# Performance work log

Hardware: AMD Instinct MI355X
Metric: run time of the kernel (lower is better)

The kernel has to match this reference:

```python
import jax, jax.numpy as jnp
import numpy as np

FEATURE_DIM = 128
HIDDEN_DIM = 128
BATCH = 500000
NEG_SLOPE = 0.2  # PyG GATConv default negative_slope


def setup_inputs() -> dict:
    key = jax.random.key(0)
    ks = jax.random.split(key, 8)
    s_in = 1.0 / np.sqrt(FEATURE_DIM)
    s_hid = 1.0 / np.sqrt(HIDDEN_DIM)
    return {
        "feature1": jax.random.normal(ks[0], (BATCH, FEATURE_DIM), jnp.float32),
        "feature2": jax.random.normal(ks[1], (BATCH, FEATURE_DIM), jnp.float32),
        # GATConv params (heads=1): lin (no bias), att_src/att_dst, output bias
        "W_gat": jax.random.normal(ks[2], (HIDDEN_DIM, FEATURE_DIM), jnp.float32) * s_in,
        "att_src": jax.random.normal(ks[3], (HIDDEN_DIM,), jnp.float32) * s_hid,
        "att_dst": jax.random.normal(ks[4], (HIDDEN_DIM,), jnp.float32) * s_hid,
        "b_gat": jnp.zeros((HIDDEN_DIM,), jnp.float32),
        # fc: Linear(hidden_dim, feature_dim)
        "W_fc": jax.random.normal(ks[5], (FEATURE_DIM, HIDDEN_DIM), jnp.float32) * s_hid,
        "b_fc": jax.random.normal(ks[6], (FEATURE_DIM,), jnp.float32) * s_hid,
    }


def _leaky_relu(x):
    return jnp.where(x > 0, x, NEG_SLOPE * x)


def reference(feature1, feature2, W_gat, att_src, att_dst, b_gat, W_fc, b_fc):
    # Per sample: 2-node graph, edges 0->1 and 1->0, plus PyG default self-loops
    # 0->0, 1->1. Vectorized over the batch.
    H1 = feature1 @ W_gat.T  # [B, hidden] = W x_0
    H2 = feature2 @ W_gat.T  # [B, hidden] = W x_1

    s1s = H1 @ att_src  # [B]
    s1d = H1 @ att_dst
    s2s = H2 @ att_src
    s2d = H2 @ att_dst

    # Destination node 0: incoming edges 1->0 and 0->0 (self-loop)
    e10 = _leaky_relu(s2s + s1d)
    e00 = _leaky_relu(s1s + s1d)
    a0 = jax.nn.softmax(jnp.stack([e10, e00], axis=-1), axis=-1)  # [B, 2]
    out0 = a0[:, 0:1] * H2 + a0[:, 1:2] * H1 + b_gat  # [B, hidden]

    # Destination node 1: incoming edges 0->1 and 1->1 (self-loop)
    e01 = _leaky_relu(s1s + s2d)
    e11 = _leaky_relu(s2s + s2d)
    a1 = jax.nn.softmax(jnp.stack([e01, e11], axis=-1), axis=-1)  # [B, 2]
    out1 = a1[:, 0:1] * H1 + a1[:, 1:2] * H2 + b_gat  # [B, hidden]

    # fc then mean over the 2 nodes; fc is affine so fc(mean) == mean(fc)
    m = 0.5 * (out0 + out1)  # [B, hidden]
    return m @ W_fc.T + b_fc  # [B, feature_dim]
```

## Files before the change

kernel.cpp:

```cpp
#include <hip/hip_runtime.h>
#include <hip/hip_bf16.h>

#define FEAT 128
#define BATCH_N 500000

typedef unsigned short u16;
typedef __attribute__((ext_vector_type(8))) short short8;

__device__ __forceinline__ u16 f2bf(float f) {
  union { float f; unsigned u; } cv; cv.f = f;
  unsigned u = cv.u;
  return (u16)((u + 0x7fffu + ((u >> 16) & 1u)) >> 16);
}

__device__ __forceinline__ float bf2f(u16 b) {
  union { unsigned u; float f; } cv; cv.u = ((unsigned)b) << 16; return cv.f;
}

__device__ __forceinline__ float lrelu(float x) { return x > 0.f ? x : 0.2f * x; }

__global__ __launch_bounds__(128) void prep_kernel(
    const float* __restrict__ Wg, const float* __restrict__ as_,
    const float* __restrict__ ad_, const float* __restrict__ bg,
    const float* __restrict__ Wf, const float* __restrict__ bf_,
    u16* __restrict__ Mbf, float* __restrict__ u, float* __restrict__ v,
    float* __restrict__ c) {
  const int i = blockIdx.x, k = threadIdx.x;
  float acc = 0.f;
  for (int j = 0; j < FEAT; ++j) acc = fmaf(Wf[i * FEAT + j], Wg[j * FEAT + k], acc);
  Mbf[i * FEAT + k] = f2bf(acc);
  if (i == 0) {
    float uu = 0.f, vv = 0.f;
    for (int j = 0; j < FEAT; ++j) {
      float w = Wg[j * FEAT + k];
      uu = fmaf(as_[j], w, uu);
      vv = fmaf(ad_[j], w, vv);
    }
    u[k] = uu; v[k] = vv;
  } else if (i == 1) {
    float cc = bf_[k];
    for (int j = 0; j < FEAT; ++j) cc = fmaf(Wf[k * FEAT + j], bg[j], cc);
    c[k] = cc;
  }
}

__global__ __launch_bounds__(256) void gat_kernel(
    const float* __restrict__ f1, const float* __restrict__ f2,
    const u16* __restrict__ Mbf, const float* __restrict__ u,
    const float* __restrict__ v, const float* __restrict__ c,
    float* __restrict__ out) {
  __shared__ __align__(16) u16 M_lds[128 * 136];
  __shared__ __align__(16) u16 x_lds[64 * 136];

  const int tid = threadIdx.x;
  const int lane = tid & 63;
  const int wave = tid >> 6;
  const int k4 = lane & 31;
  const int hlf = lane >> 5;

  const uint4* Ms = reinterpret_cast<const uint4*>(Mbf);
#pragma unroll
  for (int it = 0; it < 8; ++it) {
    int g = it * 256 + tid;
    int n = g >> 4, kc = (g & 15) << 3;
    *reinterpret_cast<uint4*>(&M_lds[n * 136 + kc]) = Ms[g];
  }

  const float4 uvec = reinterpret_cast<const float4*>(u)[k4];
  const float4 vvec = reinterpret_cast<const float4*>(v)[k4];

  __syncthreads();

  const int rbase = blockIdx.x * 64 + wave * 16;
  const bool active = rbase < BATCH_N;

  if (active) {
    const float4* f1p = reinterpret_cast<const float4*>(f1) + (size_t)rbase * 32;
    const float4* f2p = reinterpret_cast<const float4*>(f2) + (size_t)rbase * 32;
    float4 nf1 = f1p[hlf * 32 + k4];
    float4 nf2 = f2p[hlf * 32 + k4];
#pragma unroll
    for (int it = 0; it < 8; ++it) {
      float4 a1 = nf1, a2 = nf2;
      if (it < 7) {
        int o = (it * 2 + 2 + hlf) * 32 + k4;
        nf1 = f1p[o];
        nf2 = f2p[o];
      }
      float d1s = a1.x * uvec.x + a1.y * uvec.y + a1.z * uvec.z + a1.w * uvec.w;
      float d1d = a1.x * vvec.x + a1.y * vvec.y + a1.z * vvec.z + a1.w * vvec.w;
      float d2s = a2.x * uvec.x + a2.y * uvec.y + a2.z * uvec.z + a2.w * uvec.w;
      float d2d = a2.x * vvec.x + a2.y * vvec.y + a2.z * vvec.z + a2.w * vvec.w;
#pragma unroll
      for (int m = 1; m <= 16; m <<= 1) {
        d1s += __shfl_xor(d1s, m, 64);
        d1d += __shfl_xor(d1d, m, 64);
        d2s += __shfl_xor(d2s, m, 64);
        d2d += __shfl_xor(d2d, m, 64);
      }
      float e10 = lrelu(d2s + d1d);
      float e00 = lrelu(d1s + d1d);
      float mx0 = fmaxf(e10, e00);
      float p10 = __expf(e10 - mx0), p00 = __expf(e00 - mx0);
      float inv0 = 1.0f / (p10 + p00);
      float e01 = lrelu(d1s + d2d);
      float e11 = lrelu(d2s + d2d);
      float mx1 = fmaxf(e01, e11);
      float p01 = __expf(e01 - mx1), p11 = __expf(e11 - mx1);
      float inv1 = 1.0f / (p01 + p11);
      float alpha = 0.5f * (p00 * inv0 + p01 * inv1);
      float beta  = 0.5f * (p10 * inv0 + p11 * inv1);
      ushort4 xw;
      xw.x = f2bf(alpha * a1.x + beta * a2.x);
      xw.y = f2bf(alpha * a1.y + beta * a2.y);
      xw.z = f2bf(alpha * a1.z + beta * a2.z);
      xw.w = f2bf(alpha * a1.w + beta * a2.w);
      int xrow = wave * 16 + it * 2 + hlf;
      *reinterpret_cast<ushort4*>(&x_lds[xrow * 136 + k4 * 4]) = xw;
    }
  }

  __syncthreads();

  const int rg = tid >> 4;
  const int cg = tid & 15;
  float cl[8];
#pragma unroll
  for (int j = 0; j < 8; ++j) cl[j] = c[cg * 8 + j];

  float acc[4][8];
#pragma unroll
  for (int r = 0; r < 4; ++r)
#pragma unroll
    for (int j = 0; j < 8; ++j) acc[r][j] = 0.f;

  for (int kc = 0; kc < 128; kc += 8) {
    const int kr = (kc + cg * 8) & 127;
    float xf[4][8];
#pragma unroll
    for (int r = 0; r < 4; ++r) {
      short8 s = *reinterpret_cast<const short8*>(&x_lds[(rg * 4 + r) * 136 + kr]);
#pragma unroll
      for (int e = 0; e < 8; ++e) xf[r][e] = bf2f((u16)s[e]);
    }
#pragma unroll
    for (int j = 0; j < 8; ++j) {
      short8 s = *reinterpret_cast<const short8*>(&M_lds[(cg * 8 + j) * 136 + kr]);
#pragma unroll
      for (int e = 0; e < 8; ++e) {
        float mv = bf2f((u16)s[e]);
#pragma unroll
        for (int r = 0; r < 4; ++r) acc[r][j] = fmaf(xf[r][e], mv, acc[r][j]);
      }
    }
  }

  const int rowbase = blockIdx.x * 64 + rg * 4;
#pragma unroll
  for (int r = 0; r < 4; ++r) {
    int grow = rowbase + r;
    if (grow < BATCH_N) {
#pragma unroll
      for (int j = 0; j < 8; ++j) {
        out[(size_t)grow * 128 + cg * 8 + j] = acc[r][j] + cl[j];
      }
    }
  }
}

extern "C" void kernel_launch(void* const* d_in, const int* in_sizes, int n_in,
                              void* d_out, int out_size, void* d_ws, size_t ws_size,
                              hipStream_t stream) {
  const float* f1 = (const float*)d_in[0];
  const float* f2 = (const float*)d_in[1];
  const float* Wg = (const float*)d_in[2];
  const float* as_ = (const float*)d_in[3];
  const float* ad_ = (const float*)d_in[4];
  const float* bg = (const float*)d_in[5];
  const float* Wf = (const float*)d_in[6];
  const float* bf_ = (const float*)d_in[7];
  float* out = (float*)d_out;

  u16* Mbf = (u16*)d_ws;
  float* u = (float*)((char*)d_ws + 32768);
  float* v = u + 128;
  float* c = v + 128;

  prep_kernel<<<dim3(128), dim3(128), 0, stream>>>(Wg, as_, ad_, bg, Wf, bf_, Mbf, u, v, c);
  const int nblocks = (BATCH_N + 63) / 64;
  gat_kernel<<<dim3(nblocks), dim3(256), 0, stream>>>(f1, f2, Mbf, u, v, c, out);
}
```

Measured before the change: 751.8 us.

## Replace scalar FMA epilogue GEMM with bf16 MFMA 16x16x32 instructions

```diff
diff --git a/kernel.cpp b/kernel.cpp
--- a/kernel.cpp
+++ b/kernel.cpp
@@ -6,15 +6,12 @@
 
 typedef unsigned short u16;
 typedef __attribute__((ext_vector_type(8))) short short8;
+typedef __attribute__((ext_vector_type(4))) float f32x4;
 
 __device__ __forceinline__ u16 f2bf(float f) {
   union { float f; unsigned u; } cv; cv.f = f;
   unsigned u = cv.u;
   return (u16)((u + 0x7fffu + ((u >> 16) & 1u)) >> 16);
-}
-
-__device__ __forceinline__ float bf2f(u16 b) {
-  union { unsigned u; float f; } cv; cv.u = ((unsigned)b) << 16; return cv.f;
 }
 
 __device__ __forceinline__ float lrelu(float x) { return x > 0.f ? x : 0.2f * x; }
@@ -69,6 +66,12 @@
   const float4 uvec = reinterpret_cast<const float4*>(u)[k4];
   const float4 vvec = reinterpret_cast<const float4*>(v)[k4];
 
+  const int lr = lane & 15;
+  const int lk = lane >> 4;
+  float creg[8];
+#pragma unroll
+  for (int ct = 0; ct < 8; ++ct) creg[ct] = c[ct * 16 + lr];
+
   __syncthreads();
 
   const int rbase = blockIdx.x * 64 + wave * 16;
@@ -122,48 +125,28 @@
 
   __syncthreads();
 
-  const int rg = tid >> 4;
-  const int cg = tid & 15;
-  float cl[8];
+  short8 afr[4];
 #pragma unroll
-  for (int j = 0; j < 8; ++j) cl[j] = c[cg * 8 + j];
+  for (int kk = 0; kk < 4; ++kk)
+    afr[kk] = *reinterpret_cast<const short8*>(
+        &x_lds[(wave * 16 + lr) * 136 + kk * 32 + lk * 8]);
 
-  float acc[4][8];
+  const int rowbase = blockIdx.x * 64 + wave * 16 + lk * 4;
 #pragma unroll
-  for (int r = 0; r < 4; ++r)
+  for (int ct = 0; ct < 8; ++ct) {
+    f32x4 acc = {0.f, 0.f, 0.f, 0.f};
 #pragma unroll
-    for (int j = 0; j < 8; ++j) acc[r][j] = 0.f;
-
-  for (int kc = 0; kc < 128; kc += 8) {
-    const int kr = (kc + cg * 8) & 127;
-    float xf[4][8];
+    for (int kk = 0; kk < 4; ++kk) {
+      short8 bfr = *reinterpret_cast<const short8*>(
+          &M_lds[(ct * 16 + lr) * 136 + kk * 32 + lk * 8]);
+      acc = __builtin_amdgcn_mfma_f32_16x16x32_bf16(afr[kk], bfr, acc, 0, 0, 0);
+    }
+    const int gcol = ct * 16 + lr;
+    const float cj = creg[ct];
 #pragma unroll
     for (int r = 0; r < 4; ++r) {
-      short8 s = *reinterpret_cast<const short8*>(&x_lds[(rg * 4 + r) * 136 + kr]);
-#pragma unroll
-      for (int e = 0; e < 8; ++e) xf[r][e] = bf2f((u16)s[e]);
-    }
-#pragma unroll
-    for (int j = 0; j < 8; ++j) {
-      short8 s = *reinterpret_cast<const short8*>(&M_lds[(cg * 8 + j) * 136 + kr]);
-#pragma unroll
-      for (int e = 0; e < 8; ++e) {
-        float mv = bf2f((u16)s[e]);
-#pragma unroll
-        for (int r = 0; r < 4; ++r) acc[r][j] = fmaf(xf[r][e], mv, acc[r][j]);
-      }
-    }
-  }
-
-  const int rowbase = blockIdx.x * 64 + rg * 4;
-#pragma unroll
-  for (int r = 0; r < 4; ++r) {
-    int grow = rowbase + r;
-    if (grow < BATCH_N) {
-#pragma unroll
-      for (int j = 0; j < 8; ++j) {
-        out[(size_t)grow * 128 + cg * 8 + j] = acc[r][j] + cl[j];
-      }
+      const int grow = rowbase + r;
+      if (grow < BATCH_N) out[(size_t)grow * 128 + gcol] = acc[r] + cj;
     }
   }
 }
```

Result: faster. 609.6 us (-18.9%).
